# Performance work log

Measured on AMD Instinct MI355X. Metric: run time of the kernel, lower is better.

Reference implementation:

```python
import jax, jax.numpy as jnp
import numpy as np

N_NODES = 50000
N_EDGES = 800000
NUM_FEATURES = 256
HIDDEN = 128
NUM_CLASSES = 64


def gcn_conv(x, edge_index, W, b):
    """PyG-style GCNConv: out = D^-1/2 (A+I) D^-1/2 (x W) + b.

    edge_index[0] = source (j), edge_index[1] = target (i);
    messages flow source -> target and are summed at the target.
    """
    n = x.shape[0]
    loop = jnp.arange(n, dtype=edge_index.dtype)
    src = jnp.concatenate([edge_index[0], loop])  # [E+N]
    dst = jnp.concatenate([edge_index[1], loop])  # [E+N]

    h = x @ W  # [N, out_dim] — transform before propagate, as in PyG GCNConv

    deg = jax.ops.segment_sum(jnp.ones_like(dst, dtype=h.dtype), dst, num_segments=n)
    dinv = jnp.where(deg > 0, jax.lax.rsqrt(deg), 0.0)
    norm = dinv[src] * dinv[dst]  # [E+N]

    out = jax.ops.segment_sum(norm[:, None] * h[src], dst, num_segments=n)
    return out + b


def setup_inputs() -> dict:
    key = jax.random.key(0)
    k1, k2, k3, k4 = jax.random.split(key, 4)
    x = jax.random.normal(k1, (N_NODES, NUM_FEATURES), dtype=jnp.float32)
    edge_index = jax.random.randint(k2, (2, N_EDGES), 0, N_NODES, dtype=jnp.int64)
    # Glorot-style init for the two GCN layer weights, zero bias (PyG default)
    W1 = jax.random.normal(k3, (NUM_FEATURES, HIDDEN), dtype=jnp.float32) * (1.0 / np.sqrt(NUM_FEATURES))
    b1 = jnp.zeros((HIDDEN,), dtype=jnp.float32)
    W2 = jax.random.normal(k4, (HIDDEN, NUM_CLASSES), dtype=jnp.float32) * (1.0 / np.sqrt(HIDDEN))
    b2 = jnp.zeros((NUM_CLASSES,), dtype=jnp.float32)
    return {"x": x, "edge_index": edge_index, "W1": W1, "b1": b1, "W2": W2, "b2": b2}


def reference(x, edge_index, W1, b1, W2, b2):
    h = gcn_conv(x, edge_index, W1, b1)
    h = jax.nn.relu(h)
    # dropout(p=0.5, training=True): fixed key stands in for torch RNG
    keep = jax.random.bernoulli(jax.random.key(42), 0.5, h.shape)
    h = jnp.where(keep, h * 2.0, 0.0)
    out = gcn_conv(h, edge_index, W2, b2)
    return out
```

## Files before the change

kernel.cpp:

```cpp
#include <hip/hip_runtime.h>


typedef __attribute__((ext_vector_type(8))) short bf16x8;
typedef __attribute__((ext_vector_type(4))) float f32x4;
typedef __attribute__((ext_vector_type(8))) unsigned short us8;

__device__ __forceinline__ unsigned tf_rotl(unsigned x, int d) {
    return (x << d) | (x >> (32 - d));
}

__device__ __forceinline__ bool dropout_keep(unsigned flat_idx) {
    const unsigned K0 = 0u, K1 = 42u;
    const unsigned K2 = K0 ^ K1 ^ 0x1BD11BDAu;
    unsigned x0 = 0u, x1 = flat_idx;
    x0 += K0; x1 += K1;
#define TF_R(r) { x0 += x1; x1 = tf_rotl(x1, (r)); x1 ^= x0; }
    TF_R(13) TF_R(15) TF_R(26) TF_R(6)
    x0 += K1; x1 += K2 + 1u;
    TF_R(17) TF_R(29) TF_R(16) TF_R(24)
    x0 += K2; x1 += K0 + 2u;
    TF_R(13) TF_R(15) TF_R(26) TF_R(6)
    x0 += K0; x1 += K1 + 3u;
    TF_R(17) TF_R(29) TF_R(16) TF_R(24)
    x0 += K1; x1 += K2 + 4u;
    TF_R(13) TF_R(15) TF_R(26) TF_R(6)
    x0 += K2; x1 += K0 + 5u;
#undef TF_R
    return (((x0 ^ x1) >> 31) & 1u) == 0u;
}

__device__ __forceinline__ unsigned short bf16_rn(float x) {
    unsigned u = __float_as_uint(x);
    unsigned r = u + 0x7FFFu + ((u >> 16) & 1u);
    return (unsigned short)(r >> 16);
}
__device__ __forceinline__ void split_bf16(float x, unsigned short& h, unsigned short& l) {
    h = bf16_rn(x);
    float fh = __uint_as_float(((unsigned)h) << 16);
    l = bf16_rn(x - fh);
}
__device__ __forceinline__ void split4(float4 v, ushort4& h, ushort4& l) {
    unsigned short h0, h1, h2, h3, l0, l1, l2, l3;
    split_bf16(v.x, h0, l0); split_bf16(v.y, h1, l1);
    split_bf16(v.z, h2, l2); split_bf16(v.w, h3, l3);
    h = make_ushort4(h0, h1, h2, h3);
    l = make_ushort4(l0, l1, l2, l3);
}

__device__ __forceinline__ int ei_stride(const int* __restrict__ ei) {
    bool i64 = true;
#pragma unroll
    for (int k = 1; k <= 15; k += 2) i64 = i64 && (ei[k] == 0);
    return i64 ? 2 : 1;
}

template <int K_, int NOUT_, bool SPLITA>
__device__ __forceinline__ void gemm_core(const void* __restrict__ Xv,
                                          const unsigned short* __restrict__ wT_hi,
                                          const unsigned short* __restrict__ wT_lo,
                                          unsigned short* __restrict__ Yb,
                                          int nrows, int bid) {
    constexpr int BM = 64, BK = 32, NKT = K_ / BK;
    constexpr int CT = NOUT_ / 64;
    constexpr int LDW = BK + 8;

    __shared__ __attribute__((aligned(16))) unsigned short xs_hi[BM][LDW];
    __shared__ __attribute__((aligned(16))) unsigned short xs_lo[SPLITA ? BM : 1][SPLITA ? LDW : 1];

    const int t = threadIdx.x;
    const int wave = t >> 6, lane = t & 63;
    const int m16 = lane & 15, kg = lane >> 4;
    const int row0 = bid * BM;
    const int n0 = wave * (16 * CT);

    const float* Xf = (const float*)Xv;
    const unsigned short* Xb = (const unsigned short*)Xv;

    f32x4 acc[4][CT];
#pragma unroll
    for (int r = 0; r < 4; ++r)
#pragma unroll
        for (int c = 0; c < CT; ++c) acc[r][c] = {0.f, 0.f, 0.f, 0.f};

    float4 xpre[2];
    us8 xpre_b;
    bf16x8 bh[2][CT], bl[2][CT];

    if constexpr (SPLITA) {
#pragma unroll
        for (int i = 0; i < 2; ++i) {
            int idx = t + i * 256;
            int r = idx >> 3, c4 = idx & 7;
            int gr = row0 + r;
            xpre[i] = (gr < nrows) ? *(const float4*)&Xf[(size_t)gr * K_ + c4 * 4]
                                   : make_float4(0.f, 0.f, 0.f, 0.f);
        }
    } else {
        int r = t >> 2, c8 = t & 3;
        int gr = row0 + r;
        xpre_b = (gr < nrows) ? *(const us8*)&Xb[(size_t)gr * K_ + c8 * 8] : (us8)0;
    }
#pragma unroll
    for (int c = 0; c < CT; ++c) {
        const size_t wrow = (size_t)(n0 + c * 16 + m16) * K_ + kg * 8;
        bh[0][c] = *(const bf16x8*)&wT_hi[wrow];
        bl[0][c] = *(const bf16x8*)&wT_lo[wrow];
    }

#pragma unroll
    for (int kb = 0; kb < NKT; ++kb) {
        const int cur = kb & 1, nxt = cur ^ 1;
        if constexpr (SPLITA) {
#pragma unroll
            for (int i = 0; i < 2; ++i) {
                int idx = t + i * 256;
                int r = idx >> 3, c4 = idx & 7;
                ushort4 h, l;
                split4(xpre[i], h, l);
                *(ushort4*)&xs_hi[r][c4 * 4] = h;
                *(ushort4*)&xs_lo[r][c4 * 4] = l;
            }
        } else {
            int r = t >> 2, c8 = t & 3;
            *(us8*)&xs_hi[r][c8 * 8] = xpre_b;
        }
        __syncthreads();

        if (kb + 1 < NKT) {
            const int koff = (kb + 1) * BK;
            if constexpr (SPLITA) {
#pragma unroll
                for (int i = 0; i < 2; ++i) {
                    int idx = t + i * 256;
                    int r = idx >> 3, c4 = idx & 7;
                    int gr = row0 + r;
                    xpre[i] = (gr < nrows) ? *(const float4*)&Xf[(size_t)gr * K_ + koff + c4 * 4]
                                           : make_float4(0.f, 0.f, 0.f, 0.f);
                }
            } else {
                int r = t >> 2, c8 = t & 3;
                int gr = row0 + r;
                xpre_b = (gr < nrows) ? *(const us8*)&Xb[(size_t)gr * K_ + koff + c8 * 8] : (us8)0;
            }
#pragma unroll
            for (int c = 0; c < CT; ++c) {
                const size_t wrow = (size_t)(n0 + c * 16 + m16) * K_ + koff + kg * 8;
                bh[nxt][c] = *(const bf16x8*)&wT_hi[wrow];
                bl[nxt][c] = *(const bf16x8*)&wT_lo[wrow];
            }
        }

#pragma unroll
        for (int r = 0; r < 4; ++r) {
            bf16x8 ah = *(const bf16x8*)&xs_hi[r * 16 + m16][kg * 8];
            if constexpr (SPLITA) {
                bf16x8 al = *(const bf16x8*)&xs_lo[r * 16 + m16][kg * 8];
#pragma unroll
                for (int c = 0; c < CT; ++c) {
                    acc[r][c] = __builtin_amdgcn_mfma_f32_16x16x32_bf16(ah, bh[cur][c], acc[r][c], 0, 0, 0);
                    acc[r][c] = __builtin_amdgcn_mfma_f32_16x16x32_bf16(ah, bl[cur][c], acc[r][c], 0, 0, 0);
                    acc[r][c] = __builtin_amdgcn_mfma_f32_16x16x32_bf16(al, bh[cur][c], acc[r][c], 0, 0, 0);
                }
            } else {
#pragma unroll
                for (int c = 0; c < CT; ++c) {
                    acc[r][c] = __builtin_amdgcn_mfma_f32_16x16x32_bf16(ah, bh[cur][c], acc[r][c], 0, 0, 0);
                    acc[r][c] = __builtin_amdgcn_mfma_f32_16x16x32_bf16(ah, bl[cur][c], acc[r][c], 0, 0, 0);
                }
            }
        }
        __syncthreads();
    }

#pragma unroll
    for (int r = 0; r < 4; ++r) {
#pragma unroll
        for (int j = 0; j < 4; ++j) {
            int gr = row0 + r * 16 + kg * 4 + j;
            if (gr < nrows) {
#pragma unroll
                for (int c = 0; c < CT; ++c)
                    Yb[(size_t)gr * NOUT_ + n0 + c * 16 + m16] = bf16_rn(acc[r][c][j]);
            }
        }
    }
}

__global__ __launch_bounds__(256)
void prep(const float* __restrict__ W1, const float* __restrict__ W2,
          unsigned short* __restrict__ wT1_hi, unsigned short* __restrict__ wT1_lo,
          unsigned short* __restrict__ wT2_hi, unsigned short* __restrict__ wT2_lo,
          unsigned* __restrict__ deg, int N) {
    const int b = blockIdx.x, t = threadIdx.x;
    if (b < 160) {
        int idx = b * 256 + t;
        unsigned short h, l;
        if (idx < 256 * 128) {
            int k = idx / 128, n = idx % 128;
            split_bf16(W1[idx], h, l);
            wT1_hi[(size_t)n * 256 + k] = h;
            wT1_lo[(size_t)n * 256 + k] = l;
        } else if (idx < 256 * 128 + 128 * 64) {
            int j = idx - 256 * 128;
            int k = j / 64, n = j % 64;
            split_bf16(W2[j], h, l);
            wT2_hi[(size_t)n * 128 + k] = h;
            wT2_lo[(size_t)n * 128 + k] = l;
        }
    } else {
        int i = (b - 160) * 256 + t;
        if (i < N) deg[i] = 0;
    }
}

__global__ __launch_bounds__(256)
void mega1(const float* __restrict__ x, const unsigned short* __restrict__ wT1_hi,
           const unsigned short* __restrict__ wT1_lo, unsigned short* __restrict__ buffA,
           const int* __restrict__ ei, unsigned* __restrict__ deg,
           unsigned* __restrict__ aux, int N, int E, int nGemm) {
    if ((int)blockIdx.x < nGemm) {
        gemm_core<256, 128, true>(x, wT1_hi, wT1_lo, buffA, N, blockIdx.x);
        return;
    }
    int e = (blockIdx.x - nGemm) * 256 + threadIdx.x;
    if (e >= E) return;
    size_t st = ei_stride(ei);
    aux[e] = atomicAdd(&deg[ei[((size_t)E + e) * st]], 1u);
}

__global__ __launch_bounds__(256)
void scan_phase1(const unsigned* __restrict__ deg, unsigned* __restrict__ blockSums,
                 float* __restrict__ dinv, int N) {
    const int i = blockIdx.x * 256 + threadIdx.x;
    const int lane = threadIdx.x & 63, wave = threadIdx.x >> 6;
    if (blockIdx.x == 0 && threadIdx.x == 0) dinv[N] = 0.0f;
    unsigned v = 0;
    if (i < N) {
        unsigned d = deg[i];
        v = (d + 7u) & ~7u;
        dinv[i] = rsqrtf((float)(d + 1u));
    }
    unsigned s = v;
#pragma unroll
    for (int o = 32; o > 0; o >>= 1) s += __shfl_down(s, o, 64);
    __shared__ unsigned ws[4];
    if (lane == 0) ws[wave] = s;
    __syncthreads();
    if (threadIdx.x == 0)
        blockSums[blockIdx.x] = ws[0] + ws[1] + ws[2] + ws[3];
}

__global__ __launch_bounds__(256)
void scan_phase3b(const unsigned* __restrict__ deg, const unsigned* __restrict__ blockSums,
                  unsigned* __restrict__ rowptr, int* __restrict__ csr, int N, int nb) {
    __shared__ unsigned s[256];
    const int t = threadIdx.x;

    unsigned bsv = (t < nb) ? blockSums[t] : 0u;
    s[t] = bsv;
    __syncthreads();
    for (int off = 1; off < 256; off <<= 1) {
        unsigned u = (t >= off) ? s[t - off] : 0u;
        __syncthreads();
        s[t] += u;
        __syncthreads();
    }
    const unsigned off0 = (blockIdx.x == 0) ? 0u : s[blockIdx.x - 1];
    __syncthreads();

    const int i = blockIdx.x * 256 + t;
    unsigned d = 0, v = 0;
    if (i < N) { d = deg[i]; v = (d + 7u) & ~7u; }
    s[t] = v;
    __syncthreads();
    for (int off = 1; off < 256; off <<= 1) {
        unsigned u = (t >= off) ? s[t - off] : 0u;
        __syncthreads();
        s[t] += u;
        __syncthreads();
    }
    const unsigned incl = s[t];
    if (i < N) {
        const unsigned rp = off0 + incl - v;
        rowptr[i] = rp;
        if (i == N - 1) rowptr[N] = off0 + incl;
        for (unsigned u = d; u < v; ++u) csr[rp + u] = N;
    }
}

__global__ void place_edges(const int* __restrict__ ei, const unsigned* __restrict__ rowptr,
                            const unsigned* __restrict__ aux, int* __restrict__ csr, int E) {
    int e = blockIdx.x * blockDim.x + threadIdx.x;
    if (e >= E) return;
    size_t st = ei_stride(ei);
    int s = ei[(size_t)e * st];
    int d = ei[((size_t)E + e) * st];
    csr[rowptr[d] + aux[e]] = s;
}

__global__ __launch_bounds__(256)
void gemm2_kernel(const unsigned short* __restrict__ Xb, const unsigned short* __restrict__ wT_hi,
                  const unsigned short* __restrict__ wT_lo, unsigned short* __restrict__ Yb,
                  int nrows) {
    gemm_core<128, 64, false>(Xb, wT_hi, wT_lo, Yb, nrows, blockIdx.x);
}

__global__ __launch_bounds__(256)
void gather_drop(const unsigned* __restrict__ hs , const int* __restrict__ csr,
                 const unsigned* __restrict__ rowptr, const float* __restrict__ dinv,
                 const float* __restrict__ bias, unsigned* __restrict__ outb ,
                 int N) {
    const int node = blockIdx.x * 4 + (threadIdx.x >> 6);
    if (node >= N) return;
    const int lane = threadIdx.x & 63;
    const unsigned beg = rowptr[node];
    const unsigned end = rowptr[node + 1];
    const float dn = dinv[node];

    unsigned v = hs[(size_t)node * 64 + lane];
    float ax = dn * __uint_as_float(v << 16);
    float ay = dn * __uint_as_float(v & 0xffff0000u);
    for (unsigned k = beg; k < end; k += 8) {
        int j[8];
#pragma unroll
        for (int u = 0; u < 8; ++u) j[u] = csr[k + u];
        unsigned w8[8];
        float dv[8];
#pragma unroll
        for (int u = 0; u < 8; ++u) { w8[u] = hs[(size_t)j[u] * 64 + lane]; dv[u] = dinv[j[u]]; }
#pragma unroll
        for (int u = 0; u < 8; ++u) {
            ax = fmaf(dv[u], __uint_as_float(w8[u] << 16), ax);
            ay = fmaf(dv[u], __uint_as_float(w8[u] & 0xffff0000u), ay);
        }
    }
    const int f0 = 2 * lane;
    float o0 = fmaxf(fmaf(dn, ax, bias[f0]), 0.0f);
    float o1 = fmaxf(fmaf(dn, ay, bias[f0 + 1]), 0.0f);
    unsigned base = (unsigned)node * 128u + (unsigned)f0;
    o0 = dropout_keep(base) ? 2.0f * o0 : 0.0f;
    o1 = dropout_keep(base + 1u) ? 2.0f * o1 : 0.0f;
    outb[(size_t)node * 64 + lane] =
        (unsigned)bf16_rn(o0) | ((unsigned)bf16_rn(o1) << 16);
}

__global__ __launch_bounds__(256)
void gather_out(const unsigned short* __restrict__ hs , const int* __restrict__ csr,
                const unsigned* __restrict__ rowptr, const float* __restrict__ dinv,
                const float* __restrict__ bias, float* __restrict__ outp, int N) {
    const int node = blockIdx.x * 4 + (threadIdx.x >> 6);
    if (node >= N) return;
    const int lane = threadIdx.x & 63;
    const unsigned beg = rowptr[node];
    const unsigned end = rowptr[node + 1];
    const float dn = dinv[node];

    float acc = dn * __uint_as_float(((unsigned)hs[(size_t)node * 64 + lane]) << 16);
    for (unsigned k = beg; k < end; k += 8) {
        int j[8];
#pragma unroll
        for (int u = 0; u < 8; ++u) j[u] = csr[k + u];
        unsigned short w8[8];
        float dv[8];
#pragma unroll
        for (int u = 0; u < 8; ++u) { w8[u] = hs[(size_t)j[u] * 64 + lane]; dv[u] = dinv[j[u]]; }
#pragma unroll
        for (int u = 0; u < 8; ++u)
            acc = fmaf(dv[u], __uint_as_float(((unsigned)w8[u]) << 16), acc);
    }
    outp[(size_t)node * 64 + lane] = fmaf(dn, acc, bias[lane]);
}

extern "C" void kernel_launch(void* const* d_in, const int* in_sizes, int n_in,
                              void* d_out, int out_size, void* d_ws, size_t ws_size,
                              hipStream_t stream) {
    const float* x  = (const float*)d_in[0];
    const int*   ei = (const int*)d_in[1];
    const float* W1 = (const float*)d_in[2];
    const float* b1 = (const float*)d_in[3];
    const float* W2 = (const float*)d_in[4];
    const float* b2 = (const float*)d_in[5];
    float* out = (float*)d_out;

    const int Fdim = 256, Hdim = 128, Cdim = 64;
    const int N = in_sizes[0] / Fdim;
    const int E = in_sizes[1] / 2;
    const int CSR_CAP = E + 7 * N;
    const int NB = (N + 255) / 256;

    unsigned short* wT1_hi = (unsigned short*)d_ws;
    unsigned short* wT1_lo = wT1_hi + 256 * 128;
    unsigned short* wT2_hi = wT1_lo + 256 * 128;
    unsigned short* wT2_lo = wT2_hi + 128 * 64;
    unsigned short* buffA  = wT2_lo + 128 * 64;
    unsigned short* buffB  = buffA + (size_t)(N + 1) * Hdim;
    unsigned* deg    = (unsigned*)(buffB + (size_t)N * Hdim);
    float*    dinv   = (float*)(deg + N);
    unsigned* rowptr = (unsigned*)(dinv + (N + 1));
    unsigned* blockSums = rowptr + (N + 1);
    unsigned* aux    = blockSums + NB;
    int*      csr    = (int*)(aux + E);

    const int nGemm1 = (N + 63) / 64;
    const int nCount = (E + 255) / 256;

    prep<<<160 + NB, 256, 0, stream>>>(W1, W2, wT1_hi, wT1_lo, wT2_hi, wT2_lo, deg, N);
    mega1<<<nGemm1 + nCount, 256, 0, stream>>>(x, wT1_hi, wT1_lo, buffA, ei, deg, aux, N, E, nGemm1);
    scan_phase1<<<NB, 256, 0, stream>>>(deg, blockSums, dinv, N);
    scan_phase3b<<<NB, 256, 0, stream>>>(deg, blockSums, rowptr, csr, N, NB);
    place_edges<<<nCount, 256, 0, stream>>>(ei, rowptr, aux, csr, E);

    gather_drop<<<(N + 3) / 4, 256, 0, stream>>>((const unsigned*)buffA, csr, rowptr, dinv, b1,
                                                 (unsigned*)buffB, N);
    gemm2_kernel<<<(N + 63) / 64, 256, 0, stream>>>(buffB, wT2_hi, wT2_lo, buffA, N);
    gather_out<<<(N + 3) / 4, 256, 0, stream>>>(buffA, csr, rowptr, dinv, b2, out, N);
}
```

Measured before the change: 232.9 us.

## Fuse second-layer GEMM into first gather with per-wave fp32 matvec

The dense W2 multiply is folded into the first-layer gather kernel: after ReLU and dropout, each wave writes its 128-wide hidden row to shared memory and computes the 64 outputs with an fp32 dot product that reads W2 directly. This removes the separate gemm2 launch, the bf16 round trip of the hidden activations through global memory, and the W2 hi/lo split prep. In exchange each wave does 128 scalar FMAs per lane with W2 reads served from cache instead of MFMA, which may raise gather kernel compute. Precision of the hidden row improves since it is no longer rounded to bf16 before the GEMM.

```diff
diff --git a/kernel.cpp b/kernel.cpp
--- a/kernel.cpp
+++ b/kernel.cpp
@@ -54,8 +54,8 @@
     return i64 ? 2 : 1;
 }
 
-template <int K_, int NOUT_, bool SPLITA>
-__device__ __forceinline__ void gemm_core(const void* __restrict__ Xv,
+template <int K_, int NOUT_>
+__device__ __forceinline__ void gemm_core(const float* __restrict__ Xf,
                                           const unsigned short* __restrict__ wT_hi,
                                           const unsigned short* __restrict__ wT_lo,
                                           unsigned short* __restrict__ Yb,
@@ -65,7 +65,7 @@
     constexpr int LDW = BK + 8;
 
     __shared__ __attribute__((aligned(16))) unsigned short xs_hi[BM][LDW];
-    __shared__ __attribute__((aligned(16))) unsigned short xs_lo[SPLITA ? BM : 1][SPLITA ? LDW : 1];
+    __shared__ __attribute__((aligned(16))) unsigned short xs_lo[BM][LDW];
 
     const int t = threadIdx.x;
     const int wave = t >> 6, lane = t & 63;
@@ -73,9 +73,6 @@
     const int row0 = bid * BM;
     const int n0 = wave * (16 * CT);
 
-    const float* Xf = (const float*)Xv;
-    const unsigned short* Xb = (const unsigned short*)Xv;
-
     f32x4 acc[4][CT];
 #pragma unroll
     for (int r = 0; r < 4; ++r)
@@ -83,22 +80,15 @@
         for (int c = 0; c < CT; ++c) acc[r][c] = {0.f, 0.f, 0.f, 0.f};
 
     float4 xpre[2];
-    us8 xpre_b;
     bf16x8 bh[2][CT], bl[2][CT];
 
-    if constexpr (SPLITA) {
-#pragma unroll
-        for (int i = 0; i < 2; ++i) {
-            int idx = t + i * 256;
-            int r = idx >> 3, c4 = idx & 7;
-            int gr = row0 + r;
-            xpre[i] = (gr < nrows) ? *(const float4*)&Xf[(size_t)gr * K_ + c4 * 4]
-                                   : make_float4(0.f, 0.f, 0.f, 0.f);
-        }
-    } else {
-        int r = t >> 2, c8 = t & 3;
+#pragma unroll
+    for (int i = 0; i < 2; ++i) {
+        int idx = t + i * 256;
+        int r = idx >> 3, c4 = idx & 7;
         int gr = row0 + r;
-        xpre_b = (gr < nrows) ? *(const us8*)&Xb[(size_t)gr * K_ + c8 * 8] : (us8)0;
+        xpre[i] = (gr < nrows) ? *(const float4*)&Xf[(size_t)gr * K_ + c4 * 4]
+                               : make_float4(0.f, 0.f, 0.f, 0.f);
     }
 #pragma unroll
     for (int c = 0; c < CT; ++c) {
@@ -110,37 +100,26 @@
 #pragma unroll
     for (int kb = 0; kb < NKT; ++kb) {
         const int cur = kb & 1, nxt = cur ^ 1;
-        if constexpr (SPLITA) {
+#pragma unroll
+        for (int i = 0; i < 2; ++i) {
+            int idx = t + i * 256;
+            int r = idx >> 3, c4 = idx & 7;
+            ushort4 h, l;
+            split4(xpre[i], h, l);
+            *(ushort4*)&xs_hi[r][c4 * 4] = h;
+            *(ushort4*)&xs_lo[r][c4 * 4] = l;
+        }
+        __syncthreads();
+
+        if (kb + 1 < NKT) {
+            const int koff = (kb + 1) * BK;
 #pragma unroll
             for (int i = 0; i < 2; ++i) {
                 int idx = t + i * 256;
                 int r = idx >> 3, c4 = idx & 7;
-                ushort4 h, l;
-                split4(xpre[i], h, l);
-                *(ushort4*)&xs_hi[r][c4 * 4] = h;
-                *(ushort4*)&xs_lo[r][c4 * 4] = l;
-            }
-        } else {
-            int r = t >> 2, c8 = t & 3;
-            *(us8*)&xs_hi[r][c8 * 8] = xpre_b;
-        }
-        __syncthreads();
-
-        if (kb + 1 < NKT) {
-            const int koff = (kb + 1) * BK;
-            if constexpr (SPLITA) {
-#pragma unroll
-                for (int i = 0; i < 2; ++i) {
-                    int idx = t + i * 256;
-                    int r = idx >> 3, c4 = idx & 7;
-                    int gr = row0 + r;
-                    xpre[i] = (gr < nrows) ? *(const float4*)&Xf[(size_t)gr * K_ + koff + c4 * 4]
-                                           : make_float4(0.f, 0.f, 0.f, 0.f);
-                }
-            } else {
-                int r = t >> 2, c8 = t & 3;
                 int gr = row0 + r;
-                xpre_b = (gr < nrows) ? *(const us8*)&Xb[(size_t)gr * K_ + koff + c8 * 8] : (us8)0;
+                xpre[i] = (gr < nrows) ? *(const float4*)&Xf[(size_t)gr * K_ + koff + c4 * 4]
+                                       : make_float4(0.f, 0.f, 0.f, 0.f);
             }
 #pragma unroll
             for (int c = 0; c < CT; ++c) {
@@ -153,20 +132,12 @@
 #pragma unroll
         for (int r = 0; r < 4; ++r) {
             bf16x8 ah = *(const bf16x8*)&xs_hi[r * 16 + m16][kg * 8];
-            if constexpr (SPLITA) {
-                bf16x8 al = *(const bf16x8*)&xs_lo[r * 16 + m16][kg * 8];
-#pragma unroll
-                for (int c = 0; c < CT; ++c) {
-                    acc[r][c] = __builtin_amdgcn_mfma_f32_16x16x32_bf16(ah, bh[cur][c], acc[r][c], 0, 0, 0);
-                    acc[r][c] = __builtin_amdgcn_mfma_f32_16x16x32_bf16(ah, bl[cur][c], acc[r][c], 0, 0, 0);
-                    acc[r][c] = __builtin_amdgcn_mfma_f32_16x16x32_bf16(al, bh[cur][c], acc[r][c], 0, 0, 0);
-                }
-            } else {
-#pragma unroll
-                for (int c = 0; c < CT; ++c) {
-                    acc[r][c] = __builtin_amdgcn_mfma_f32_16x16x32_bf16(ah, bh[cur][c], acc[r][c], 0, 0, 0);
-                    acc[r][c] = __builtin_amdgcn_mfma_f32_16x16x32_bf16(ah, bl[cur][c], acc[r][c], 0, 0, 0);
-                }
+            bf16x8 al = *(const bf16x8*)&xs_lo[r * 16 + m16][kg * 8];
+#pragma unroll
+            for (int c = 0; c < CT; ++c) {
+                acc[r][c] = __builtin_amdgcn_mfma_f32_16x16x32_bf16(ah, bh[cur][c], acc[r][c], 0, 0, 0);
+                acc[r][c] = __builtin_amdgcn_mfma_f32_16x16x32_bf16(ah, bl[cur][c], acc[r][c], 0, 0, 0);
+                acc[r][c] = __builtin_amdgcn_mfma_f32_16x16x32_bf16(al, bh[cur][c], acc[r][c], 0, 0, 0);
             }
         }
         __syncthreads();
@@ -187,28 +158,19 @@
 }
 
 __global__ __launch_bounds__(256)
-void prep(const float* __restrict__ W1, const float* __restrict__ W2,
+void prep(const float* __restrict__ W1,
           unsigned short* __restrict__ wT1_hi, unsigned short* __restrict__ wT1_lo,
-          unsigned short* __restrict__ wT2_hi, unsigned short* __restrict__ wT2_lo,
           unsigned* __restrict__ deg, int N) {
     const int b = blockIdx.x, t = threadIdx.x;
-    if (b < 160) {
+    if (b < 128) {
         int idx = b * 256 + t;
+        int k = idx / 128, n = idx % 128;
         unsigned short h, l;
-        if (idx < 256 * 128) {
-            int k = idx / 128, n = idx % 128;
-            split_bf16(W1[idx], h, l);
-            wT1_hi[(size_t)n * 256 + k] = h;
-            wT1_lo[(size_t)n * 256 + k] = l;
-        } else if (idx < 256 * 128 + 128 * 64) {
-            int j = idx - 256 * 128;
-            int k = j / 64, n = j % 64;
-            split_bf16(W2[j], h, l);
-            wT2_hi[(size_t)n * 128 + k] = h;
-            wT2_lo[(size_t)n * 128 + k] = l;
-        }
+        split_bf16(W1[idx], h, l);
+        wT1_hi[(size_t)n * 256 + k] = h;
+        wT1_lo[(size_t)n * 256 + k] = l;
     } else {
-        int i = (b - 160) * 256 + t;
+        int i = (b - 128) * 256 + t;
         if (i < N) deg[i] = 0;
     }
 }
@@ -219,7 +181,7 @@
            const int* __restrict__ ei, unsigned* __restrict__ deg,
            unsigned* __restrict__ aux, int N, int E, int nGemm) {
     if ((int)blockIdx.x < nGemm) {
-        gemm_core<256, 128, true>(x, wT1_hi, wT1_lo, buffA, N, blockIdx.x);
+        gemm_core<256, 128>(x, wT1_hi, wT1_lo, buffA, N, blockIdx.x);
         return;
     }
     int e = (blockIdx.x - nGemm) * 256 + threadIdx.x;
@@ -299,18 +261,13 @@
 }
 
 __global__ __launch_bounds__(256)
-void gemm2_kernel(const unsigned short* __restrict__ Xb, const unsigned short* __restrict__ wT_hi,
-                  const unsigned short* __restrict__ wT_lo, unsigned short* __restrict__ Yb,
-                  int nrows) {
-    gemm_core<128, 64, false>(Xb, wT_hi, wT_lo, Yb, nrows, blockIdx.x);
-}
-
-__global__ __launch_bounds__(256)
-void gather_drop(const unsigned* __restrict__ hs , const int* __restrict__ csr,
-                 const unsigned* __restrict__ rowptr, const float* __restrict__ dinv,
-                 const float* __restrict__ bias, unsigned* __restrict__ outb ,
-                 int N) {
-    const int node = blockIdx.x * 4 + (threadIdx.x >> 6);
+void gather_fused(const unsigned* __restrict__ hs , const int* __restrict__ csr,
+                  const unsigned* __restrict__ rowptr, const float* __restrict__ dinv,
+                  const float* __restrict__ bias, const float* __restrict__ W2,
+                  unsigned short* __restrict__ gout, int N) {
+    __shared__ float h2s[4][128];
+    const int wv = threadIdx.x >> 6;
+    const int node = blockIdx.x * 4 + wv;
     if (node >= N) return;
     const int lane = threadIdx.x & 63;
     const unsigned beg = rowptr[node];
@@ -340,8 +297,21 @@
     unsigned base = (unsigned)node * 128u + (unsigned)f0;
     o0 = dropout_keep(base) ? 2.0f * o0 : 0.0f;
     o1 = dropout_keep(base + 1u) ? 2.0f * o1 : 0.0f;
-    outb[(size_t)node * 64 + lane] =
-        (unsigned)bf16_rn(o0) | ((unsigned)bf16_rn(o1) << 16);
+
+    ((float2*)h2s[wv])[lane] = make_float2(o0, o1);
+
+    float g = 0.0f;
+    const float4* h4p = (const float4*)h2s[wv];
+#pragma unroll 4
+    for (int k4 = 0; k4 < 32; ++k4) {
+        float4 h4 = h4p[k4];
+        const float* wp = &W2[(size_t)(k4 * 4) * 64 + lane];
+        g = fmaf(h4.x, wp[0], g);
+        g = fmaf(h4.y, wp[64], g);
+        g = fmaf(h4.z, wp[128], g);
+        g = fmaf(h4.w, wp[192], g);
+    }
+    gout[(size_t)node * 64 + lane] = bf16_rn(g);
 }
 
 __global__ __launch_bounds__(256)
@@ -390,11 +360,9 @@
 
     unsigned short* wT1_hi = (unsigned short*)d_ws;
     unsigned short* wT1_lo = wT1_hi + 256 * 128;
-    unsigned short* wT2_hi = wT1_lo + 256 * 128;
-    unsigned short* wT2_lo = wT2_hi + 128 * 64;
-    unsigned short* buffA  = wT2_lo + 128 * 64;
-    unsigned short* buffB  = buffA + (size_t)(N + 1) * Hdim;
-    unsigned* deg    = (unsigned*)(buffB + (size_t)N * Hdim);
+    unsigned short* buffA  = wT1_lo + 256 * 128;
+    unsigned short* buffG  = buffA + (size_t)(N + 1) * Hdim;
+    unsigned* deg    = (unsigned*)(buffG + (size_t)(N + 1) * Cdim);
     float*    dinv   = (float*)(deg + N);
     unsigned* rowptr = (unsigned*)(dinv + (N + 1));
     unsigned* blockSums = rowptr + (N + 1);
@@ -404,14 +372,13 @@
     const int nGemm1 = (N + 63) / 64;
     const int nCount = (E + 255) / 256;
 
-    prep<<<160 + NB, 256, 0, stream>>>(W1, W2, wT1_hi, wT1_lo, wT2_hi, wT2_lo, deg, N);
+    prep<<<128 + NB, 256, 0, stream>>>(W1, wT1_hi, wT1_lo, deg, N);
     mega1<<<nGemm1 + nCount, 256, 0, stream>>>(x, wT1_hi, wT1_lo, buffA, ei, deg, aux, N, E, nGemm1);
     scan_phase1<<<NB, 256, 0, stream>>>(deg, blockSums, dinv, N);
     scan_phase3b<<<NB, 256, 0, stream>>>(deg, blockSums, rowptr, csr, N, NB);
     place_edges<<<nCount, 256, 0, stream>>>(ei, rowptr, aux, csr, E);
 
-    gather_drop<<<(N + 3) / 4, 256, 0, stream>>>((const unsigned*)buffA, csr, rowptr, dinv, b1,
-                                                 (unsigned*)buffB, N);
-    gemm2_kernel<<<(N + 63) / 64, 256, 0, stream>>>(buffB, wT2_hi, wT2_lo, buffA, N);
-    gather_out<<<(N + 3) / 4, 256, 0, stream>>>(buffA, csr, rowptr, dinv, b2, out, N);
-}
+    gather_fused<<<(N + 3) / 4, 256, 0, stream>>>((const unsigned*)buffA, csr, rowptr, dinv, b1,
+                                                  W2, buffG, N);
+    gather_out<<<(N + 3) / 4, 256, 0, stream>>>(buffG, csr, rowptr, dinv, b2, out, N);
+}
```

Result: slower. 262.1 us (+12.5%).
